# Kernel optimization log

Measured on AMD Instinct MI355X. Metric: run time of the kernel, lower is better.

Reference implementation:

```python
import jax, jax.numpy as jnp
import numpy as np

N, E, D, H, L, G = 50000, 800000, 128, 8, 3, 64
C = D // H  # per-head dim


def setup_inputs() -> dict:
    key = jax.random.key(0)
    ks = jax.random.split(key, 10)
    s = 1.0 / np.sqrt(D)  # glorot-ish scale
    return {
        "x": jax.random.normal(ks[0], (N, D), jnp.float32),
        "edge_index": jax.random.randint(ks[1], (2, E), 0, N, jnp.int32),
        "batch": jnp.sort(jax.random.randint(ks[2], (N,), 0, G, jnp.int32)),
        "Wq": jax.random.normal(ks[3], (L, D, D), jnp.float32) * s,
        "bq": jnp.zeros((L, D), jnp.float32),
        "Wk": jax.random.normal(ks[4], (L, D, D), jnp.float32) * s,
        "bk": jnp.zeros((L, D), jnp.float32),
        "Wv": jax.random.normal(ks[5], (L, D, D), jnp.float32) * s,
        "bv": jnp.zeros((L, D), jnp.float32),
        "Ws": jax.random.normal(ks[6], (L, D, D), jnp.float32) * s,
        "bs": jnp.zeros((L, D), jnp.float32),
        "w_gate": jax.random.normal(ks[7], (D, 1), jnp.float32) * s,
        "b_gate": jnp.zeros((1,), jnp.float32),
    }


def transformer_conv(x, src, dst, Wq, bq, Wk, bk, Wv, bv, Ws, bs):
    # PyG TransformerConv (concat=True, root_weight=True, no edge_attr, eval mode)
    n = x.shape[0]
    q = (x @ Wq + bq).reshape(n, H, C)
    k = (x @ Wk + bk).reshape(n, H, C)
    v = (x @ Wv + bv).reshape(n, H, C)
    # attention logits per edge: [E, H]
    alpha = jnp.einsum('ehc,ehc->eh', q[dst], k[src]) / np.sqrt(C).astype(np.float32)
    # segment softmax over incoming edges of each destination node
    amax = jax.ops.segment_max(alpha, dst, num_segments=n)          # [N, H]
    ea = jnp.exp(alpha - amax[dst])
    denom = jax.ops.segment_sum(ea, dst, num_segments=n)            # [N, H]
    attn = ea / (denom[dst] + 1e-16)                                # [E, H]
    msg = v[src] * attn[:, :, None]                                 # [E, H, C]
    out = jax.ops.segment_sum(msg, dst, num_segments=n).reshape(n, H * C)
    return out + x @ Ws + bs                                        # skip connection


def reference(x, edge_index, batch, Wq, bq, Wk, bk, Wv, bv, Ws, bs, w_gate, b_gate):
    src, dst = edge_index[0], edge_index[1]
    for l in range(L):
        x = transformer_conv(x, src, dst, Wq[l], bq[l], Wk[l], bk[l],
                             Wv[l], bv[l], Ws[l], bs[l])
    # ReadoutPhase: gated sum pool || max pool
    score = jax.nn.sigmoid(x @ w_gate + b_gate)                     # [N, 1]
    pool_sum = jax.ops.segment_sum(score * x, batch, num_segments=G)
    pool_max = jax.ops.segment_max(x, batch, num_segments=G)
    return jnp.concatenate([pool_sum, pool_max], axis=1)            # [G, 2D]
```

## Files before the change

### kernel.cpp

```cpp
#include <hip/hip_runtime.h>
#include <hip/hip_bf16.h>

#define NN 50000
#define EE 800000
#define GG 64
#define PCH 16
#define SCB ((NN + 255) / 256)

typedef __attribute__((ext_vector_type(8)))  short          s16x8;
typedef __attribute__((ext_vector_type(8)))  unsigned short u16x8;
typedef __attribute__((ext_vector_type(16))) float          f32x16;

union BFU { __hip_bfloat16 h; unsigned short u; };
__device__ __forceinline__ unsigned short f2bf(float f) {
    BFU b; b.h = __float2bfloat16(f); return b.u;
}
#define B2F_LO(u) __uint_as_float((u) << 16)
#define B2F_HI(u) __uint_as_float((u) & 0xffff0000u)
#define BF2F(us)  __uint_as_float(((unsigned)(us)) << 16)

__global__ __launch_bounds__(256) void hist_kernel(const int* __restrict__ dst,
                                                   int* __restrict__ counts) {
    int e = blockIdx.x * 256 + threadIdx.x;
    if (e < EE) atomicAdd(&counts[dst[e]], 1);
}

__global__ __launch_bounds__(256)
void block_scan(const int* __restrict__ counts, int* __restrict__ offsets,
                int* __restrict__ bsums) {
    __shared__ int sm[256];
    const int t = threadIdx.x;
    const int i = blockIdx.x * 256 + t;
    const int v = (i < NN) ? counts[i] : 0;
    sm[t] = v;
    __syncthreads();
    for (int off = 1; off < 256; off <<= 1) {
        int val = (t >= off) ? sm[t - off] : 0;
        __syncthreads();
        sm[t] += val;
        __syncthreads();
    }
    if (i < NN) offsets[i] = sm[t] - v;
    if (t == 255) bsums[blockIdx.x] = sm[255];
}

__global__ __launch_bounds__(256)
void scan_sums(int* __restrict__ bsums) {
    __shared__ int sm[256];
    const int t = threadIdx.x;
    const int v = (t < SCB) ? bsums[t] : 0;
    sm[t] = v;
    __syncthreads();
    for (int off = 1; off < 256; off <<= 1) {
        int val = (t >= off) ? sm[t - off] : 0;
        __syncthreads();
        sm[t] += val;
        __syncthreads();
    }
    if (t < SCB) bsums[t] = sm[t] - v;
}

__global__ __launch_bounds__(256)
void add_base(int* __restrict__ offsets, const int* __restrict__ bsums) {
    const int i = blockIdx.x * 256 + threadIdx.x;
    if (i < NN) offsets[i] += bsums[blockIdx.x];
    if (i == 0) offsets[NN] = EE;
}

__global__ __launch_bounds__(256) void scatter_kernel(const int* __restrict__ src,
                                                      const int* __restrict__ dst,
                                                      const int* __restrict__ offs,
                                                      int* __restrict__ cursor,
                                                      int* __restrict__ csrc) {
    int e = blockIdx.x * 256 + threadIdx.x;
    if (e < EE) {
        int dn = dst[e];
        int p = atomicAdd(&cursor[dn], 1);
        csrc[offs[dn] + p] = src[e];
    }
}

__global__ __launch_bounds__(256) void starts_kernel(const int* __restrict__ batch,
                                                     int* __restrict__ starts) {
    int i = blockIdx.x * 256 + threadIdx.x;
    if (i > NN) return;
    int b  = (i < NN) ? batch[i] : GG;
    int bp = (i == 0) ? -1 : batch[i - 1];
    for (int g = bp + 1; g <= b && g <= GG; ++g) starts[g] = i;
}

__global__ __launch_bounds__(256)
void deg_hist(const int* __restrict__ counts, int* __restrict__ dhist) {
    __shared__ int lh[256];
    const int t = threadIdx.x;
    lh[t] = 0;
    __syncthreads();
    const int i = blockIdx.x * 256 + t;
    if (i < NN) atomicAdd(&lh[min(counts[i], 255)], 1);
    __syncthreads();
    if (lh[t]) atomicAdd(&dhist[t], lh[t]);
}

__global__ __launch_bounds__(256)
void deg_scan(int* __restrict__ dhist) {
    __shared__ int sm[256];
    const int t = threadIdx.x;
    const int v = dhist[t];
    sm[t] = v;
    __syncthreads();
    for (int off = 1; off < 256; off <<= 1) {
        int val = (t >= off) ? sm[t - off] : 0;
        __syncthreads();
        sm[t] += val;
        __syncthreads();
    }
    dhist[t] = sm[t] - v;
}

__global__ __launch_bounds__(256)
void deg_scatter(const int* __restrict__ counts, const int* __restrict__ dbase,
                 int* __restrict__ dcur, int* __restrict__ perm) {
    __shared__ int lh[256];
    __shared__ int lb[256];
    const int t = threadIdx.x;
    lh[t] = 0;
    __syncthreads();
    const int i = blockIdx.x * 256 + t;
    int d = 0, r = 0;
    if (i < NN) {
        d = min(counts[i], 255);
        r = atomicAdd(&lh[d], 1);
    }
    __syncthreads();
    if (lh[t]) lb[t] = atomicAdd(&dcur[t], lh[t]);
    __syncthreads();
    if (i < NN) perm[dbase[d] + lb[d] + r] = i;
}

__global__ __launch_bounds__(256)
void prep_weights(const float* __restrict__ Wq, const float* __restrict__ Wk,
                  const float* __restrict__ Wv, const float* __restrict__ Ws,
                  unsigned short* __restrict__ wfh, unsigned short* __restrict__ wfl) {
    const int mat = blockIdx.x;
    const int l = mat >> 2, m = mat & 3;
    const float* W;
    switch (m) {
        case 0:  W = Wq; break;
        case 1:  W = Wk; break;
        case 2:  W = Wv; break;
        default: W = Ws; break;
    }
    W += (size_t)l * 16384;
    const int t = threadIdx.x;
    const int col = blockIdx.y * 16 + (t >> 4);
    const int kk  = t & 15;
    u16x8 hi, lo;
    #pragma unroll
    for (int j = 0; j < 8; ++j) {
        float w = W[(kk * 8 + j) * 128 + col];
        unsigned short uh = f2bf(w);
        hi[j] = uh;
        lo[j] = f2bf(w - BF2F(uh));
    }
    const size_t o = (size_t)mat * 16384 + ((size_t)kk * 128 + col) * 8;
    *(u16x8*)(wfh + o) = hi;
    *(u16x8*)(wfl + o) = lo;
}

__global__ __launch_bounds__(256)
void gemm_mfma(const float* __restrict__ xin,
               const unsigned short* __restrict__ wHg,
               const unsigned short* __restrict__ wLg,
               const float* __restrict__ bq, const float* __restrict__ bk,
               const float* __restrict__ bv, const float* __restrict__ bs,
               float* __restrict__ q, unsigned short* __restrict__ kvb,
               float* __restrict__ xs) {
    __shared__ unsigned short xl[16384];
    const int t = threadIdx.x;
    const int n0 = blockIdx.x * 64;

    const float4* X4 = (const float4*)xin;
    for (int i = t; i < 1024; i += 256) {
        const int row = i >> 4, ch = i & 15;
        const int node = n0 + row;
        float4 fa = make_float4(0.f, 0.f, 0.f, 0.f);
        float4 fb = make_float4(0.f, 0.f, 0.f, 0.f);
        if (node < NN) { fa = X4[node * 32 + ch * 2]; fb = X4[node * 32 + ch * 2 + 1]; }
        const float fv[8] = {fa.x, fa.y, fa.z, fa.w, fb.x, fb.y, fb.z, fb.w};
        u16x8 hi, lo;
        #pragma unroll
        for (int j = 0; j < 8; ++j) {
            unsigned short uh = f2bf(fv[j]);
            hi[j] = uh;
            lo[j] = f2bf(fv[j] - BF2F(uh));
        }
        const int base = row * 128 + (ch ^ (row & 7)) * 8;
        *(u16x8*)&xl[base] = hi;
        *(u16x8*)&xl[8192 + base] = lo;
    }
    __syncthreads();

    const int lane = t & 63, wid = t >> 6;
    const int r = lane & 31, g = lane >> 5;
    const int nt = (wid & 1) * 32;
    const int cb = (wid >> 1) * 64;
    s16x8 ah[8], al[8];
    {
        const int row = nt + r;
        const int s = row & 7;
        const int rb = row * 128;
        #pragma unroll
        for (int kc = 0; kc < 8; ++kc) {
            const int idx = rb + (((kc << 1) | g) ^ s) * 8;
            ah[kc] = *(const s16x8*)&xl[idx];
            al[kc] = *(const s16x8*)&xl[8192 + idx];
        }
    }
    const int col0 = cb + r, col1 = cb + 32 + r;

    #pragma unroll
    for (int m = 0; m < 4; ++m) {
        const bool split = (m == 0 || m == 3);
        const unsigned short* WH = wHg + m * 16384;
        const unsigned short* WL = wLg + m * 16384;
        f32x16 acc0, acc1;
        #pragma unroll
        for (int j = 0; j < 16; ++j) { acc0[j] = 0.f; acc1[j] = 0.f; }

        #pragma unroll
        for (int kc = 0; kc < 8; ++kc) {
            const int kk = (kc << 1) | g;
            const s16x8 b0 = *(const s16x8*)&WH[(kk * 128 + col0) * 8];
            const s16x8 b1 = *(const s16x8*)&WH[(kk * 128 + col1) * 8];
            acc0 = __builtin_amdgcn_mfma_f32_32x32x16_bf16(ah[kc], b0, acc0, 0, 0, 0);
            acc1 = __builtin_amdgcn_mfma_f32_32x32x16_bf16(ah[kc], b1, acc1, 0, 0, 0);
            if (split) {
                acc0 = __builtin_amdgcn_mfma_f32_32x32x16_bf16(al[kc], b0, acc0, 0, 0, 0);
                acc1 = __builtin_amdgcn_mfma_f32_32x32x16_bf16(al[kc], b1, acc1, 0, 0, 0);
                const s16x8 c0 = *(const s16x8*)&WL[(kk * 128 + col0) * 8];
                const s16x8 c1 = *(const s16x8*)&WL[(kk * 128 + col1) * 8];
                acc0 = __builtin_amdgcn_mfma_f32_32x32x16_bf16(ah[kc], c0, acc0, 0, 0, 0);
                acc1 = __builtin_amdgcn_mfma_f32_32x32x16_bf16(ah[kc], c1, acc1, 0, 0, 0);
            }
        }

        const float* bp;
        switch (m) {
            case 0:  bp = bq; break;
            case 1:  bp = bk; break;
            case 2:  bp = bv; break;
            default: bp = bs; break;
        }
        const float b0 = bp[col0], b1 = bp[col1];
        if (m == 0 || m == 3) {
            float* outp = (m == 0) ? q : xs;
            #pragma unroll
            for (int reg = 0; reg < 16; ++reg) {
                const int node = n0 + nt + (reg & 3) + 8 * (reg >> 2) + 4 * g;
                if (node < NN) {
                    outp[node * 128 + col0] = acc0[reg] + b0;
                    outp[node * 128 + col1] = acc1[reg] + b1;
                }
            }
        } else {
            const int koff = (m == 1) ? 0 : 16;
            const int o0 = (col0 >> 4) * 32 + koff + (col0 & 15);
            const int o1 = (col1 >> 4) * 32 + koff + (col1 & 15);
            #pragma unroll
            for (int reg = 0; reg < 16; ++reg) {
                const int node = n0 + nt + (reg & 3) + 8 * (reg >> 2) + 4 * g;
                if (node < NN) {
                    kvb[(size_t)node * 256 + o0] = f2bf(acc0[reg] + b0);
                    kvb[(size_t)node * 256 + o1] = f2bf(acc1[reg] + b1);
                }
            }
        }
    }
}

__global__ __launch_bounds__(256)
void attn_kernel(const float* __restrict__ q, const uint4* __restrict__ kv4,
                 float* __restrict__ xio,
                 const int* __restrict__ offs, const int* __restrict__ csrc,
                 const int* __restrict__ perm) {
    const int t = threadIdx.x;
    const int h = t & 7;
    const int quarter = (t >> 3) & 3;
    const int idx = blockIdx.x * 8 + (t >> 5);
    const int n = perm[NN - 1 - idx];
    const float4* qp = (const float4*)(q + n * 128 + h * 16);
    const float4 q0 = qp[0], q1 = qp[1], q2 = qp[2], q3 = qp[3];
    float m = -__builtin_inff();
    float d = 0.f;
    float4 a0 = {}, a1 = {}, a2 = {}, a3 = {};
    const int e0 = offs[n], e1 = offs[n + 1];
    const int estart = e0 + quarter;
    if (estart < e1) {
        uint4 ka, kb, va, vb;
        { const uint4* p = kv4 + (size_t)csrc[estart] * 32 + h * 4;
          ka = p[0]; kb = p[1]; va = p[2]; vb = p[3]; }
        uint4 na, nb, nc, nd;
        if (estart + 4 < e1) {
            const uint4* p = kv4 + (size_t)csrc[estart + 4] * 32 + h * 4;
            na = p[0]; nb = p[1]; nc = p[2]; nd = p[3];
        }
        for (int ec = estart; ec < e1; ec += 4) {
            uint4 fa, fb, fc, fd;
            if (ec + 8 < e1) {
                const uint4* p = kv4 + (size_t)csrc[ec + 8] * 32 + h * 4;
                fa = p[0]; fb = p[1]; fc = p[2]; fd = p[3];
            }
            float dot =
                q0.x * B2F_LO(ka.x) + q0.y * B2F_HI(ka.x) + q0.z * B2F_LO(ka.y) + q0.w * B2F_HI(ka.y)
              + q1.x * B2F_LO(ka.z) + q1.y * B2F_HI(ka.z) + q1.z * B2F_LO(ka.w) + q1.w * B2F_HI(ka.w)
              + q2.x * B2F_LO(kb.x) + q2.y * B2F_HI(kb.x) + q2.z * B2F_LO(kb.y) + q2.w * B2F_HI(kb.y)
              + q3.x * B2F_LO(kb.z) + q3.y * B2F_HI(kb.z) + q3.z * B2F_LO(kb.w) + q3.w * B2F_HI(kb.w);
            const float alpha = dot * 0.25f;
            const float nm = fmaxf(m, alpha);
            const float scale = __expf(m - nm);
            const float p = __expf(alpha - nm);
            d = d * scale + p;
            a0.x = a0.x * scale + p * B2F_LO(va.x); a0.y = a0.y * scale + p * B2F_HI(va.x);
            a0.z = a0.z * scale + p * B2F_LO(va.y); a0.w = a0.w * scale + p * B2F_HI(va.y);
            a1.x = a1.x * scale + p * B2F_LO(va.z); a1.y = a1.y * scale + p * B2F_HI(va.z);
            a1.z = a1.z * scale + p * B2F_LO(va.w); a1.w = a1.w * scale + p * B2F_HI(va.w);
            a2.x = a2.x * scale + p * B2F_LO(vb.x); a2.y = a2.y * scale + p * B2F_HI(vb.x);
            a2.z = a2.z * scale + p * B2F_LO(vb.y); a2.w = a2.w * scale + p * B2F_HI(vb.y);
            a3.x = a3.x * scale + p * B2F_LO(vb.z); a3.y = a3.y * scale + p * B2F_HI(vb.z);
            a3.z = a3.z * scale + p * B2F_LO(vb.w); a3.w = a3.w * scale + p * B2F_HI(vb.w);
            m = nm;
            ka = na; kb = nb; va = nc; vb = nd;
            na = fa; nb = fb; nc = fc; nd = fd;
        }
    }
    #pragma unroll
    for (int o = 8; o <= 16; o <<= 1) {
        const float mp = __shfl_xor(m, o);
        const float dp = __shfl_xor(d, o);
        const float mc = fmaxf(fmaxf(m, mp), -1e30f);
        const float s0 = __expf(m - mc);
        const float s1 = __expf(mp - mc);
        d = d * s0 + dp * s1;
        float pa;
        pa = __shfl_xor(a0.x, o); a0.x = a0.x * s0 + pa * s1;
        pa = __shfl_xor(a0.y, o); a0.y = a0.y * s0 + pa * s1;
        pa = __shfl_xor(a0.z, o); a0.z = a0.z * s0 + pa * s1;
        pa = __shfl_xor(a0.w, o); a0.w = a0.w * s0 + pa * s1;
        pa = __shfl_xor(a1.x, o); a1.x = a1.x * s0 + pa * s1;
        pa = __shfl_xor(a1.y, o); a1.y = a1.y * s0 + pa * s1;
        pa = __shfl_xor(a1.z, o); a1.z = a1.z * s0 + pa * s1;
        pa = __shfl_xor(a1.w, o); a1.w = a1.w * s0 + pa * s1;
        pa = __shfl_xor(a2.x, o); a2.x = a2.x * s0 + pa * s1;
        pa = __shfl_xor(a2.y, o); a2.y = a2.y * s0 + pa * s1;
        pa = __shfl_xor(a2.z, o); a2.z = a2.z * s0 + pa * s1;
        pa = __shfl_xor(a2.w, o); a2.w = a2.w * s0 + pa * s1;
        pa = __shfl_xor(a3.x, o); a3.x = a3.x * s0 + pa * s1;
        pa = __shfl_xor(a3.y, o); a3.y = a3.y * s0 + pa * s1;
        pa = __shfl_xor(a3.z, o); a3.z = a3.z * s0 + pa * s1;
        pa = __shfl_xor(a3.w, o); a3.w = a3.w * s0 + pa * s1;
        m = mc;
    }
    if (quarter == 0) {
        const float inv = 1.f / (d + 1e-16f);
        float4* op = (float4*)(xio + n * 128 + h * 16);
        float4 o0 = op[0], o1 = op[1], o2 = op[2], o3 = op[3];
        o0.x += a0.x * inv; o0.y += a0.y * inv; o0.z += a0.z * inv; o0.w += a0.w * inv;
        o1.x += a1.x * inv; o1.y += a1.y * inv; o1.z += a1.z * inv; o1.w += a1.w * inv;
        o2.x += a2.x * inv; o2.y += a2.y * inv; o2.z += a2.z * inv; o2.w += a2.w * inv;
        o3.x += a3.x * inv; o3.y += a3.y * inv; o3.z += a3.z * inv; o3.w += a3.w * inv;
        op[0] = o0; op[1] = o1; op[2] = o2; op[3] = o3;
    }
}

__global__ __launch_bounds__(128)
void pool_partial(const float* __restrict__ x, const float* __restrict__ wg,
                  const float* __restrict__ bg, const int* __restrict__ starts,
                  float* __restrict__ psum, float* __restrict__ pmax) {
    const int g  = blockIdx.x / PCH;
    const int ch = blockIdx.x % PCH;
    const int c  = threadIdx.x;
    const int s0 = starts[g], s1 = starts[g + 1];
    const int total = s1 - s0;
    const int len = (total + PCH - 1) / PCH;
    const int n0 = s0 + ch * len;
    const int n1 = min(n0 + len, s1);
    const float w = wg[c];
    const float b = bg[0];
    __shared__ float red[2];
    float sum = 0.f, mx = -__builtin_inff();
    for (int n = n0; n < n1; ++n) {
        const float xv = x[n * 128 + c];
        float p = xv * w;
        #pragma unroll
        for (int o = 32; o; o >>= 1) p += __shfl_xor(p, o);
        if ((c & 63) == 0) red[c >> 6] = p;
        __syncthreads();
        const float dot = red[0] + red[1];
        __syncthreads();
        const float score = 1.f / (1.f + __expf(-(dot + b)));
        sum += score * xv;
        mx = fmaxf(mx, xv);
    }
    psum[blockIdx.x * 128 + c] = sum;
    pmax[blockIdx.x * 128 + c] = mx;
}

__global__ __launch_bounds__(128)
void pool_final(const float* __restrict__ psum, const float* __restrict__ pmax,
                float* __restrict__ out) {
    const int g = blockIdx.x, c = threadIdx.x;
    float s = 0.f, m = -__builtin_inff();
    #pragma unroll
    for (int ch = 0; ch < PCH; ++ch) {
        s += psum[(g * PCH + ch) * 128 + c];
        m = fmaxf(m, pmax[(g * PCH + ch) * 128 + c]);
    }
    out[g * 256 + c] = s;
    out[g * 256 + 128 + c] = m;
}

extern "C" void kernel_launch(void* const* d_in, const int* in_sizes, int n_in,
                              void* d_out, int out_size, void* d_ws, size_t ws_size,
                              hipStream_t stream) {
    const float* x     = (const float*)d_in[0];
    const int*   ei    = (const int*)d_in[1];
    const int*   batch = (const int*)d_in[2];
    const float* Wq = (const float*)d_in[3];
    const float* bq = (const float*)d_in[4];
    const float* Wk = (const float*)d_in[5];
    const float* bk = (const float*)d_in[6];
    const float* Wv = (const float*)d_in[7];
    const float* bv = (const float*)d_in[8];
    const float* Ws = (const float*)d_in[9];
    const float* bs = (const float*)d_in[10];
    const float* wg = (const float*)d_in[11];
    const float* bg = (const float*)d_in[12];
    float* out = (float*)d_out;

    char* w = (char*)d_ws;
    float* qb            = (float*)w;          w += (size_t)NN * 128 * 4;
    unsigned short* kvb  = (unsigned short*)w; w += (size_t)NN * 256 * 2;
    float* bufA          = (float*)w;          w += (size_t)NN * 128 * 4;
    float* bufB          = (float*)w;          w += (size_t)NN * 128 * 4;
    float* psum          = (float*)w;          w += (size_t)GG * PCH * 128 * 4;
    float* pmax          = (float*)w;          w += (size_t)GG * PCH * 128 * 4;
    unsigned short* wfh  = (unsigned short*)w; w += (size_t)12 * 16384 * 2;
    unsigned short* wfl  = (unsigned short*)w; w += (size_t)12 * 16384 * 2;
    int* counts          = (int*)w;            w += (size_t)NN * 4;
    int* offsets         = (int*)w;            w += (size_t)(NN + 1) * 4;
    int* bsums           = (int*)w;            w += (size_t)256 * 4;
    int* dhist           = (int*)w;            w += (size_t)256 * 4;
    int* dcur            = (int*)w;            w += (size_t)256 * 4;
    int* perm            = (int*)w;            w += (size_t)NN * 4;
    int* csrc            = (int*)w;            w += (size_t)EE * 4;
    int* starts          = (int*)w;            w += (size_t)(GG + 1) * 4;

    const int* srcI = ei;
    const int* dstI = ei + EE;

    hipMemsetAsync(counts, 0, (size_t)NN * 4, stream);
    hipMemsetAsync(dhist, 0, 256 * 4, stream);
    hipMemsetAsync(dcur, 0, 256 * 4, stream);
    hist_kernel<<<(EE + 255) / 256, 256, 0, stream>>>(dstI, counts);
    block_scan<<<SCB, 256, 0, stream>>>(counts, offsets, bsums);
    scan_sums<<<1, 256, 0, stream>>>(bsums);
    add_base<<<SCB, 256, 0, stream>>>(offsets, bsums);
    deg_hist<<<SCB, 256, 0, stream>>>(counts, dhist);
    deg_scan<<<1, 256, 0, stream>>>(dhist);
    deg_scatter<<<SCB, 256, 0, stream>>>(counts, dhist, dcur, perm);
    hipMemsetAsync(counts, 0, (size_t)NN * 4, stream);
    scatter_kernel<<<(EE + 255) / 256, 256, 0, stream>>>(srcI, dstI, offsets, counts, csrc);
    starts_kernel<<<(NN + 256) / 256, 256, 0, stream>>>(batch, starts);
    prep_weights<<<dim3(12, 8), 256, 0, stream>>>(Wq, Wk, Wv, Ws, wfh, wfl);

    const float* xin = x;
    float* bufs[2] = {bufA, bufB};
    const int gemmBlocks = (NN + 63) / 64;
    const int attnBlocks = NN / 8;
    for (int l = 0; l < 3; ++l) {
        float* xs = bufs[l & 1];
        gemm_mfma<<<gemmBlocks, 256, 0, stream>>>(
            xin, wfh + (size_t)l * 4 * 16384, wfl + (size_t)l * 4 * 16384,
            bq + (size_t)l * 128, bk + (size_t)l * 128,
            bv + (size_t)l * 128, bs + (size_t)l * 128,
            qb, kvb, xs);
        attn_kernel<<<attnBlocks, 256, 0, stream>>>(qb, (const uint4*)kvb, xs, offsets, csrc, perm);
        xin = xs;
    }

    pool_partial<<<GG * PCH, 128, 0, stream>>>(xin, wg, bg, starts, psum, pmax);
    pool_final<<<GG, 128, 0, stream>>>(psum, pmax, out);
}
```

Measured before the change: 477.3 us.

## Fuse CSR preprocessing kernels and restructure K/V projection into joint pass

Merges the degree histogram into the block scan, runs both small scans in one two-block launch, folds the graph-start computation into add_base, and replaces three memsets plus a second counts reset with a single memset over a contiguous zeroed region that now holds a separate scatter cursor. This cuts the number of launches in the preprocessing chain. In the GEMM, Q and the skip projection keep the split-precision path, while K and V are computed together in one loop with four accumulators and written interleaved. This raises register pressure in exchange for better MFMA interleaving and fewer loop passes.

```diff
diff --git a/kernel.cpp b/kernel.cpp
--- a/kernel.cpp
+++ b/kernel.cpp
@@ -26,14 +26,17 @@
 }
 
 __global__ __launch_bounds__(256)
-void block_scan(const int* __restrict__ counts, int* __restrict__ offsets,
-                int* __restrict__ bsums) {
+void block_scan_deg(const int* __restrict__ counts, int* __restrict__ offsets,
+                    int* __restrict__ bsums, int* __restrict__ dhist) {
     __shared__ int sm[256];
+    __shared__ int lh[256];
     const int t = threadIdx.x;
     const int i = blockIdx.x * 256 + t;
     const int v = (i < NN) ? counts[i] : 0;
+    lh[t] = 0;
     sm[t] = v;
     __syncthreads();
+    if (i < NN) atomicAdd(&lh[min(v, 255)], 1);
     for (int off = 1; off < 256; off <<= 1) {
         int val = (t >= off) ? sm[t - off] : 0;
         __syncthreads();
@@ -42,13 +45,16 @@
     }
     if (i < NN) offsets[i] = sm[t] - v;
     if (t == 255) bsums[blockIdx.x] = sm[255];
-}
-
-__global__ __launch_bounds__(256)
-void scan_sums(int* __restrict__ bsums) {
+    if (lh[t]) atomicAdd(&dhist[t], lh[t]);
+}
+
+__global__ __launch_bounds__(256)
+void scan2(int* __restrict__ bsums, int* __restrict__ dhist) {
+    int* arr = (blockIdx.x == 0) ? bsums : dhist;
+    const int lim = (blockIdx.x == 0) ? SCB : 256;
     __shared__ int sm[256];
     const int t = threadIdx.x;
-    const int v = (t < SCB) ? bsums[t] : 0;
+    const int v = (t < lim) ? arr[t] : 0;
     sm[t] = v;
     __syncthreads();
     for (int off = 1; off < 256; off <<= 1) {
@@ -57,14 +63,40 @@
         sm[t] += val;
         __syncthreads();
     }
-    if (t < SCB) bsums[t] = sm[t] - v;
-}
-
-__global__ __launch_bounds__(256)
-void add_base(int* __restrict__ offsets, const int* __restrict__ bsums) {
+    if (t < lim) arr[t] = sm[t] - v;
+}
+
+__global__ __launch_bounds__(256)
+void add_base_starts(int* __restrict__ offsets, const int* __restrict__ bsums,
+                     const int* __restrict__ batch, int* __restrict__ starts) {
     const int i = blockIdx.x * 256 + threadIdx.x;
     if (i < NN) offsets[i] += bsums[blockIdx.x];
     if (i == 0) offsets[NN] = EE;
+    if (i <= NN) {
+        int b  = (i < NN) ? batch[i] : GG;
+        int bp = (i == 0) ? -1 : batch[i - 1];
+        for (int g = bp + 1; g <= b && g <= GG; ++g) starts[g] = i;
+    }
+}
+
+__global__ __launch_bounds__(256)
+void deg_scatter(const int* __restrict__ counts, const int* __restrict__ dbase,
+                 int* __restrict__ dcur, int* __restrict__ perm) {
+    __shared__ int lh[256];
+    __shared__ int lb[256];
+    const int t = threadIdx.x;
+    lh[t] = 0;
+    __syncthreads();
+    const int i = blockIdx.x * 256 + t;
+    int d = 0, r = 0;
+    if (i < NN) {
+        d = min(counts[i], 255);
+        r = atomicAdd(&lh[d], 1);
+    }
+    __syncthreads();
+    if (lh[t]) lb[t] = atomicAdd(&dcur[t], lh[t]);
+    __syncthreads();
+    if (i < NN) perm[dbase[d] + lb[d] + r] = i;
 }
 
 __global__ __launch_bounds__(256) void scatter_kernel(const int* __restrict__ src,
@@ -78,63 +110,6 @@
         int p = atomicAdd(&cursor[dn], 1);
         csrc[offs[dn] + p] = src[e];
     }
-}
-
-__global__ __launch_bounds__(256) void starts_kernel(const int* __restrict__ batch,
-                                                     int* __restrict__ starts) {
-    int i = blockIdx.x * 256 + threadIdx.x;
-    if (i > NN) return;
-    int b  = (i < NN) ? batch[i] : GG;
-    int bp = (i == 0) ? -1 : batch[i - 1];
-    for (int g = bp + 1; g <= b && g <= GG; ++g) starts[g] = i;
-}
-
-__global__ __launch_bounds__(256)
-void deg_hist(const int* __restrict__ counts, int* __restrict__ dhist) {
-    __shared__ int lh[256];
-    const int t = threadIdx.x;
-    lh[t] = 0;
-    __syncthreads();
-    const int i = blockIdx.x * 256 + t;
-    if (i < NN) atomicAdd(&lh[min(counts[i], 255)], 1);
-    __syncthreads();
-    if (lh[t]) atomicAdd(&dhist[t], lh[t]);
-}
-
-__global__ __launch_bounds__(256)
-void deg_scan(int* __restrict__ dhist) {
-    __shared__ int sm[256];
-    const int t = threadIdx.x;
-    const int v = dhist[t];
-    sm[t] = v;
-    __syncthreads();
-    for (int off = 1; off < 256; off <<= 1) {
-        int val = (t >= off) ? sm[t - off] : 0;
-        __syncthreads();
-        sm[t] += val;
-        __syncthreads();
-    }
-    dhist[t] = sm[t] - v;
-}
-
-__global__ __launch_bounds__(256)
-void deg_scatter(const int* __restrict__ counts, const int* __restrict__ dbase,
-                 int* __restrict__ dcur, int* __restrict__ perm) {
-    __shared__ int lh[256];
-    __shared__ int lb[256];
-    const int t = threadIdx.x;
-    lh[t] = 0;
-    __syncthreads();
-    const int i = blockIdx.x * 256 + t;
-    int d = 0, r = 0;
-    if (i < NN) {
-        d = min(counts[i], 255);
-        r = atomicAdd(&lh[d], 1);
-    }
-    __syncthreads();
-    if (lh[t]) lb[t] = atomicAdd(&dcur[t], lh[t]);
-    __syncthreads();
-    if (i < NN) perm[dbase[d] + lb[d] + r] = i;
 }
 
 __global__ __launch_bounds__(256)
@@ -219,60 +194,71 @@
     const int col0 = cb + r, col1 = cb + 32 + r;
 
     #pragma unroll
-    for (int m = 0; m < 4; ++m) {
-        const bool split = (m == 0 || m == 3);
+    for (int pm = 0; pm < 2; ++pm) {
+        const int m = pm ? 3 : 0;
         const unsigned short* WH = wHg + m * 16384;
         const unsigned short* WL = wLg + m * 16384;
         f32x16 acc0, acc1;
         #pragma unroll
         for (int j = 0; j < 16; ++j) { acc0[j] = 0.f; acc1[j] = 0.f; }
-
         #pragma unroll
         for (int kc = 0; kc < 8; ++kc) {
             const int kk = (kc << 1) | g;
             const s16x8 b0 = *(const s16x8*)&WH[(kk * 128 + col0) * 8];
             const s16x8 b1 = *(const s16x8*)&WH[(kk * 128 + col1) * 8];
+            const s16x8 c0 = *(const s16x8*)&WL[(kk * 128 + col0) * 8];
+            const s16x8 c1 = *(const s16x8*)&WL[(kk * 128 + col1) * 8];
             acc0 = __builtin_amdgcn_mfma_f32_32x32x16_bf16(ah[kc], b0, acc0, 0, 0, 0);
             acc1 = __builtin_amdgcn_mfma_f32_32x32x16_bf16(ah[kc], b1, acc1, 0, 0, 0);
-            if (split) {
-                acc0 = __builtin_amdgcn_mfma_f32_32x32x16_bf16(al[kc], b0, acc0, 0, 0, 0);
-                acc1 = __builtin_amdgcn_mfma_f32_32x32x16_bf16(al[kc], b1, acc1, 0, 0, 0);
-                const s16x8 c0 = *(const s16x8*)&WL[(kk * 128 + col0) * 8];
-                const s16x8 c1 = *(const s16x8*)&WL[(kk * 128 + col1) * 8];
-                acc0 = __builtin_amdgcn_mfma_f32_32x32x16_bf16(ah[kc], c0, acc0, 0, 0, 0);
-                acc1 = __builtin_amdgcn_mfma_f32_32x32x16_bf16(ah[kc], c1, acc1, 0, 0, 0);
+            acc0 = __builtin_amdgcn_mfma_f32_32x32x16_bf16(al[kc], b0, acc0, 0, 0, 0);
+            acc1 = __builtin_amdgcn_mfma_f32_32x32x16_bf16(al[kc], b1, acc1, 0, 0, 0);
+            acc0 = __builtin_amdgcn_mfma_f32_32x32x16_bf16(ah[kc], c0, acc0, 0, 0, 0);
+            acc1 = __builtin_amdgcn_mfma_f32_32x32x16_bf16(ah[kc], c1, acc1, 0, 0, 0);
+        }
+        const float* bp = pm ? bs : bq;
+        float* outp = pm ? xs : q;
+        const float b0 = bp[col0], b1 = bp[col1];
+        #pragma unroll
+        for (int reg = 0; reg < 16; ++reg) {
+            const int node = n0 + nt + (reg & 3) + 8 * (reg >> 2) + 4 * g;
+            if (node < NN) {
+                outp[node * 128 + col0] = acc0[reg] + b0;
+                outp[node * 128 + col1] = acc1[reg] + b1;
             }
         }
-
-        const float* bp;
-        switch (m) {
-            case 0:  bp = bq; break;
-            case 1:  bp = bk; break;
-            case 2:  bp = bv; break;
-            default: bp = bs; break;
-        }
-        const float b0 = bp[col0], b1 = bp[col1];
-        if (m == 0 || m == 3) {
-            float* outp = (m == 0) ? q : xs;
-            #pragma unroll
-            for (int reg = 0; reg < 16; ++reg) {
-                const int node = n0 + nt + (reg & 3) + 8 * (reg >> 2) + 4 * g;
-                if (node < NN) {
-                    outp[node * 128 + col0] = acc0[reg] + b0;
-                    outp[node * 128 + col1] = acc1[reg] + b1;
-                }
-            }
-        } else {
-            const int koff = (m == 1) ? 0 : 16;
-            const int o0 = (col0 >> 4) * 32 + koff + (col0 & 15);
-            const int o1 = (col1 >> 4) * 32 + koff + (col1 & 15);
-            #pragma unroll
-            for (int reg = 0; reg < 16; ++reg) {
-                const int node = n0 + nt + (reg & 3) + 8 * (reg >> 2) + 4 * g;
-                if (node < NN) {
-                    kvb[(size_t)node * 256 + o0] = f2bf(acc0[reg] + b0);
-                    kvb[(size_t)node * 256 + o1] = f2bf(acc1[reg] + b1);
-                }
+    }
+
+    {
+        const unsigned short* WK = wHg + 1 * 16384;
+        const unsigned short* WV = wHg + 2 * 16384;
+        f32x16 ak0, ak1, av0, av1;
+        #pragma unroll
+        for (int j = 0; j < 16; ++j) { ak0[j] = 0.f; ak1[j] = 0.f; av0[j] = 0.f; av1[j] = 0.f; }
+        #pragma unroll
+        for (int kc = 0; kc < 8; ++kc) {
+            const int kk = (kc << 1) | g;
+            const s16x8 k0 = *(const s16x8*)&WK[(kk * 128 + col0) * 8];
+            const s16x8 k1 = *(const s16x8*)&WK[(kk * 128 + col1) * 8];
+            const s16x8 v0 = *(const s16x8*)&WV[(kk * 128 + col0) * 8];
+            const s16x8 v1 = *(const s16x8*)&WV[(kk * 128 + col1) * 8];
+            ak0 = __builtin_amdgcn_mfma_f32_32x32x16_bf16(ah[kc], k0, ak0, 0, 0, 0);
+            ak1 = __builtin_amdgcn_mfma_f32_32x32x16_bf16(ah[kc], k1, ak1, 0, 0, 0);
+            av0 = __builtin_amdgcn_mfma_f32_32x32x16_bf16(ah[kc], v0, av0, 0, 0, 0);
+            av1 = __builtin_amdgcn_mfma_f32_32x32x16_bf16(ah[kc], v1, av1, 0, 0, 0);
+        }
+        const float bk0 = bk[col0], bk1 = bk[col1];
+        const float bv0 = bv[col0], bv1 = bv[col1];
+        const int k0o = (col0 >> 4) * 32 + (col0 & 15);
+        const int k1o = (col1 >> 4) * 32 + (col1 & 15);
+        #pragma unroll
+        for (int reg = 0; reg < 16; ++reg) {
+            const int node = n0 + nt + (reg & 3) + 8 * (reg >> 2) + 4 * g;
+            if (node < NN) {
+                unsigned short* row = kvb + (size_t)node * 256;
+                row[k0o]      = f2bf(ak0[reg] + bk0);
+                row[k1o]      = f2bf(ak1[reg] + bk1);
+                row[k0o + 16] = f2bf(av0[reg] + bv0);
+                row[k1o + 16] = f2bf(av1[reg] + bv1);
             }
         }
     }
@@ -447,10 +433,12 @@
     unsigned short* wfh  = (unsigned short*)w; w += (size_t)12 * 16384 * 2;
     unsigned short* wfl  = (unsigned short*)w; w += (size_t)12 * 16384 * 2;
     int* counts          = (int*)w;            w += (size_t)NN * 4;
+    int* cursor          = (int*)w;            w += (size_t)NN * 4;
+    int* dhist           = (int*)w;            w += (size_t)256 * 4;
+    int* dcur            = (int*)w;            w += (size_t)256 * 4;
+    const size_t zero_bytes = (size_t)(NN + NN + 256 + 256) * 4;
     int* offsets         = (int*)w;            w += (size_t)(NN + 1) * 4;
     int* bsums           = (int*)w;            w += (size_t)256 * 4;
-    int* dhist           = (int*)w;            w += (size_t)256 * 4;
-    int* dcur            = (int*)w;            w += (size_t)256 * 4;
     int* perm            = (int*)w;            w += (size_t)NN * 4;
     int* csrc            = (int*)w;            w += (size_t)EE * 4;
     int* starts          = (int*)w;            w += (size_t)(GG + 1) * 4;
@@ -458,19 +446,13 @@
     const int* srcI = ei;
     const int* dstI = ei + EE;
 
-    hipMemsetAsync(counts, 0, (size_t)NN * 4, stream);
-    hipMemsetAsync(dhist, 0, 256 * 4, stream);
-    hipMemsetAsync(dcur, 0, 256 * 4, stream);
+    hipMemsetAsync(counts, 0, zero_bytes, stream);
     hist_kernel<<<(EE + 255) / 256, 256, 0, stream>>>(dstI, counts);
-    block_scan<<<SCB, 256, 0, stream>>>(counts, offsets, bsums);
-    scan_sums<<<1, 256, 0, stream>>>(bsums);
-    add_base<<<SCB, 256, 0, stream>>>(offsets, bsums);
-    deg_hist<<<SCB, 256, 0, stream>>>(counts, dhist);
-    deg_scan<<<1, 256, 0, stream>>>(dhist);
+    block_scan_deg<<<SCB, 256, 0, stream>>>(counts, offsets, bsums, dhist);
+    scan2<<<2, 256, 0, stream>>>(bsums, dhist);
+    add_base_starts<<<SCB, 256, 0, stream>>>(offsets, bsums, batch, starts);
     deg_scatter<<<SCB, 256, 0, stream>>>(counts, dhist, dcur, perm);
-    hipMemsetAsync(counts, 0, (size_t)NN * 4, stream);
-    scatter_kernel<<<(EE + 255) / 256, 256, 0, stream>>>(srcI, dstI, offsets, counts, csrc);
-    starts_kernel<<<(NN + 256) / 256, 256, 0, stream>>>(batch, starts);
+    scatter_kernel<<<(EE + 255) / 256, 256, 0, stream>>>(srcI, dstI, offsets, cursor, csrc);
     prep_weights<<<dim3(12, 8), 256, 0, stream>>>(Wq, Wk, Wv, Ws, wfh, wfl);
 
     const float* xin = x;
```

Result: faster. 442.5 us (-7.3%).
